# Kernel optimization log

Hardware: AMD Instinct MI355X
Metric: run time of the kernel (lower is better)

## Reference

```python
import jax, jax.numpy as jnp
import numpy as np


def setup_inputs() -> dict:
    key = jax.random.key(0)
    k1, k2, k3 = jax.random.split(key, 3)
    B, S, H = 32, 2048, 1024
    hidden = jax.random.normal(k1, (B, H), dtype=jnp.float32)
    encoder_outputs = jax.random.normal(k2, (B, S, H), dtype=jnp.float32)
    W_in = jax.random.normal(k3, (H, H), dtype=jnp.float32) * (1.0 / np.sqrt(H))
    return {"hidden": hidden, "encoder_outputs": encoder_outputs, "W_in": W_in}


def reference(hidden, encoder_outputs, W_in):
    # linear_in: nn.Linear(H, H, bias=False) -> hidden @ W_in.T  [B, H]
    h = hidden @ W_in.T
    # scores: bmm(encoder_outputs [B,S,H], h [B,H,1]) -> [B,S]
    scores = jnp.einsum("bsh,bh->bs", encoder_outputs, h)
    attn_w = jax.nn.softmax(scores, axis=-1)  # [B, S]
    # context: bmm(attn_w [B,1,S], encoder_outputs [B,S,H]) -> [B, H]
    context = jnp.einsum("bs,bsh->bh", attn_w, encoder_outputs)
    return (context, attn_w)
```

## Files before the change

kernel.cpp:

```cpp
#include <hip/hip_runtime.h>
#include <math.h>

constexpr int Bb = 32;
constexpr int Ss = 2048;
constexpr int Hh = 1024;
constexpr int SC = 64;
constexpr int CPB = Ss / SC;
constexpr int NBLK = Bb * CPB;

__global__ __launch_bounds__(256) void gemv_h_kernel(const float* __restrict__ hidden,
                                                     const float* __restrict__ W,
                                                     float* __restrict__ h)
{
    int tid  = threadIdx.x;
    int wave = tid >> 6;
    int lane = tid & 63;
    int i  = blockIdx.x & (Hh - 1);
    int bg = blockIdx.x >> 10;
    int b  = bg * 4 + wave;
    const float4* wr = reinterpret_cast<const float4*>(W + (size_t)i * Hh);
    const float4* hd = reinterpret_cast<const float4*>(hidden + (size_t)b * Hh);
    float d = 0.f;
#pragma unroll
    for (int k = 0; k < 4; ++k) {
        float4 wv = wr[lane + 64 * k];
        float4 hv = hd[lane + 64 * k];
        d += wv.x * hv.x + wv.y * hv.y + wv.z * hv.z + wv.w * hv.w;
    }
#pragma unroll
    for (int off = 32; off > 0; off >>= 1) d += __shfl_xor(d, off, 64);
    if (lane == 0) h[(size_t)b * Hh + i] = d;
}

__global__ __launch_bounds__(256) void attn_partial_kernel(const float* __restrict__ enc,
                                                           const float* __restrict__ h,
                                                           float* __restrict__ scores,
                                                           float* __restrict__ pm,
                                                           float* __restrict__ pl,
                                                           float* __restrict__ pctx)
{
    int blk   = blockIdx.x;
    int b     = blk / CPB;
    int chunk = blk % CPB;
    int s0    = chunk * SC;
    int tid   = threadIdx.x;
    int wave  = tid >> 6;
    int lane  = tid & 63;

    float4 hf[4];
    const float4* h4 = reinterpret_cast<const float4*>(h + (size_t)b * Hh);
#pragma unroll
    for (int k = 0; k < 4; ++k) hf[k] = h4[lane + 64 * k];

    float m = -INFINITY;
    float l = 0.f;
    float4 ctx[4];
#pragma unroll
    for (int k = 0; k < 4; ++k) ctx[k] = make_float4(0.f, 0.f, 0.f, 0.f);

    const float4* ebase = reinterpret_cast<const float4*>(enc + ((size_t)b * Ss + s0 + wave * 16) * Hh);

#pragma unroll 2
    for (int r2 = 0; r2 < 8; ++r2) {
        const float4* eA = ebase + (size_t)(2 * r2) * (Hh / 4);
        const float4* eB = eA + (Hh / 4);
        float4 ea[4], eb[4];
#pragma unroll
        for (int k = 0; k < 4; ++k) ea[k] = eA[lane + 64 * k];
#pragma unroll
        for (int k = 0; k < 4; ++k) eb[k] = eB[lane + 64 * k];

        float d0 = 0.f, d1 = 0.f;
#pragma unroll
        for (int k = 0; k < 4; ++k) {
            d0 += ea[k].x * hf[k].x + ea[k].y * hf[k].y + ea[k].z * hf[k].z + ea[k].w * hf[k].w;
            d1 += eb[k].x * hf[k].x + eb[k].y * hf[k].y + eb[k].z * hf[k].z + eb[k].w * hf[k].w;
        }
#pragma unroll
        for (int off = 32; off > 0; off >>= 1) {
            d0 += __shfl_xor(d0, off, 64);
            d1 += __shfl_xor(d1, off, 64);
        }
        int s = s0 + wave * 16 + 2 * r2;
        if (lane == 0) {
            *reinterpret_cast<float2*>(scores + (size_t)b * Ss + s) = make_float2(d0, d1);
        }

        float mn = fmaxf(fmaxf(d0, d1), m);
        if (mn > m) {
            float c = __expf(m - mn);
            l *= c;
#pragma unroll
            for (int k = 0; k < 4; ++k) {
                ctx[k].x *= c; ctx[k].y *= c; ctx[k].z *= c; ctx[k].w *= c;
            }
            m = mn;
        }
        float p0 = __expf(d0 - m);
        float p1 = __expf(d1 - m);
        l += p0 + p1;
#pragma unroll
        for (int k = 0; k < 4; ++k) {
            ctx[k].x += p0 * ea[k].x + p1 * eb[k].x;
            ctx[k].y += p0 * ea[k].y + p1 * eb[k].y;
            ctx[k].z += p0 * ea[k].z + p1 * eb[k].z;
            ctx[k].w += p0 * ea[k].w + p1 * eb[k].w;
        }
    }

    __shared__ float lds_ctx[4][Hh];
    __shared__ float lds_m[4], lds_l[4];
    float4* ldsrow = reinterpret_cast<float4*>(lds_ctx[wave]);
#pragma unroll
    for (int k = 0; k < 4; ++k) ldsrow[64 * k + lane] = ctx[k];
    if (lane == 0) { lds_m[wave] = m; lds_l[wave] = l; }
    __syncthreads();

    float M = fmaxf(fmaxf(lds_m[0], lds_m[1]), fmaxf(lds_m[2], lds_m[3]));
    float L = 0.f;
    float4 acc = make_float4(0.f, 0.f, 0.f, 0.f);
#pragma unroll
    for (int w = 0; w < 4; ++w) {
        float c = __expf(lds_m[w] - M);
        L += c * lds_l[w];
        float4 v = reinterpret_cast<float4*>(lds_ctx[w])[tid];
        acc.x += c * v.x; acc.y += c * v.y; acc.z += c * v.z; acc.w += c * v.w;
    }
    reinterpret_cast<float4*>(pctx + (size_t)blk * Hh)[tid] = acc;
    if (tid == 0) { pm[blk] = M; pl[blk] = L; }
}

__global__ __launch_bounds__(256) void combine_finish_kernel(const float* __restrict__ pm,
                                                             const float* __restrict__ pl,
                                                             const float* __restrict__ pctx,
                                                             const float* __restrict__ scores,
                                                             float* __restrict__ out_ctx,
                                                             float* __restrict__ attn_out)
{
    int blk = blockIdx.x;
    int tid = threadIdx.x;
    if (blk < 128) {
        int b = blk >> 2;
        int col = (blk & 3) * 256 + tid;
        const float* mrow = pm + (size_t)b * CPB;
        const float* lrow = pl + (size_t)b * CPB;
        float M = -INFINITY;
#pragma unroll
        for (int c = 0; c < CPB; ++c) M = fmaxf(M, mrow[c]);
        float e[CPB];
        float L = 0.f;
#pragma unroll
        for (int c = 0; c < CPB; ++c) {
            e[c] = __expf(mrow[c] - M);
            L += e[c] * lrow[c];
        }
        float acc = 0.f;
#pragma unroll 4
        for (int c = 0; c < CPB; ++c)
            acc += e[c] * pctx[((size_t)b * CPB + c) * Hh + col];
        out_ctx[(size_t)b * Hh + col] = acc / L;
    } else {
        int idx = (blk - 128) * 256 + tid;
        int b = idx >> 11;
        const float* mrow = pm + (size_t)b * CPB;
        const float* lrow = pl + (size_t)b * CPB;
        float M = -INFINITY;
#pragma unroll
        for (int c = 0; c < CPB; ++c) M = fmaxf(M, mrow[c]);
        float L = 0.f;
#pragma unroll
        for (int c = 0; c < CPB; ++c) L += __expf(mrow[c] - M) * lrow[c];
        attn_out[idx] = __expf(scores[idx] - M) / L;
    }
}

extern "C" void kernel_launch(void* const* d_in, const int* in_sizes, int n_in,
                              void* d_out, int out_size, void* d_ws, size_t ws_size,
                              hipStream_t stream) {
    const float* hidden = (const float*)d_in[0];
    const float* enc    = (const float*)d_in[1];
    const float* W_in   = (const float*)d_in[2];

    float* out_ctx  = (float*)d_out;
    float* out_attn = (float*)d_out + Bb * Hh;

    float* ws     = (float*)d_ws;
    float* h      = ws;
    float* scores = ws + 32768;
    float* pm     = ws + 98304;
    float* pl     = ws + 99328;
    float* pctx   = ws + 100352;
    (void)in_sizes; (void)n_in; (void)out_size; (void)ws_size;

    gemv_h_kernel<<<Hh * (Bb / 4), 256, 0, stream>>>(hidden, W_in, h);
    attn_partial_kernel<<<NBLK, 256, 0, stream>>>(enc, h, scores, pm, pl, pctx);
    combine_finish_kernel<<<128 + (Bb * Ss) / 256, 256, 0, stream>>>(pm, pl, pctx, scores,
                                                                     out_ctx, out_attn);
}
```

Baseline: 64.03 us.

## Double-buffer encoder row loads and double the sequence chunk per block

Each attention block now handles 128 sequence rows instead of 64, and each wave processes groups of 4 rows. A software pipeline ping-pongs between two register buffers so the next group's loads are in flight while the current group is computed. The aim is to hide memory latency on the bandwidth-bound encoder stream and halve the partial-context traffic for the combine step. The cost is much higher register pressure (32 float4 buffers), which may lower occupancy, and fewer blocks (512).

```diff
diff --git a/kernel.cpp b/kernel.cpp
--- a/kernel.cpp
+++ b/kernel.cpp
@@ -4,7 +4,7 @@
 constexpr int Bb = 32;
 constexpr int Ss = 2048;
 constexpr int Hh = 1024;
-constexpr int SC = 64;
+constexpr int SC = 128;
 constexpr int CPB = Ss / SC;
 constexpr int NBLK = Bb * CPB;
 
@@ -40,8 +40,8 @@
                                                            float* __restrict__ pctx)
 {
     int blk   = blockIdx.x;
-    int b     = blk / CPB;
-    int chunk = blk % CPB;
+    int b     = blk >> 4;
+    int chunk = blk & (CPB - 1);
     int s0    = chunk * SC;
     int tid   = threadIdx.x;
     int wave  = tid >> 6;
@@ -58,55 +58,79 @@
 #pragma unroll
     for (int k = 0; k < 4; ++k) ctx[k] = make_float4(0.f, 0.f, 0.f, 0.f);
 
-    const float4* ebase = reinterpret_cast<const float4*>(enc + ((size_t)b * Ss + s0 + wave * 16) * Hh);
-
-#pragma unroll 2
-    for (int r2 = 0; r2 < 8; ++r2) {
-        const float4* eA = ebase + (size_t)(2 * r2) * (Hh / 4);
-        const float4* eB = eA + (Hh / 4);
-        float4 ea[4], eb[4];
-#pragma unroll
-        for (int k = 0; k < 4; ++k) ea[k] = eA[lane + 64 * k];
-#pragma unroll
-        for (int k = 0; k < 4; ++k) eb[k] = eB[lane + 64 * k];
-
-        float d0 = 0.f, d1 = 0.f;
-#pragma unroll
-        for (int k = 0; k < 4; ++k) {
-            d0 += ea[k].x * hf[k].x + ea[k].y * hf[k].y + ea[k].z * hf[k].z + ea[k].w * hf[k].w;
-            d1 += eb[k].x * hf[k].x + eb[k].y * hf[k].y + eb[k].z * hf[k].z + eb[k].w * hf[k].w;
-        }
-#pragma unroll
-        for (int off = 32; off > 0; off >>= 1) {
-            d0 += __shfl_xor(d0, off, 64);
-            d1 += __shfl_xor(d1, off, 64);
-        }
-        int s = s0 + wave * 16 + 2 * r2;
-        if (lane == 0) {
-            *reinterpret_cast<float2*>(scores + (size_t)b * Ss + s) = make_float2(d0, d1);
-        }
-
-        float mn = fmaxf(fmaxf(d0, d1), m);
-        if (mn > m) {
-            float c = __expf(m - mn);
-            l *= c;
-#pragma unroll
-            for (int k = 0; k < 4; ++k) {
-                ctx[k].x *= c; ctx[k].y *= c; ctx[k].z *= c; ctx[k].w *= c;
-            }
-            m = mn;
-        }
-        float p0 = __expf(d0 - m);
-        float p1 = __expf(d1 - m);
-        l += p0 + p1;
-#pragma unroll
-        for (int k = 0; k < 4; ++k) {
-            ctx[k].x += p0 * ea[k].x + p1 * eb[k].x;
-            ctx[k].y += p0 * ea[k].y + p1 * eb[k].y;
-            ctx[k].z += p0 * ea[k].z + p1 * eb[k].z;
-            ctx[k].w += p0 * ea[k].w + p1 * eb[k].w;
-        }
-    }
+    const float4* ebase = reinterpret_cast<const float4*>(enc + ((size_t)b * Ss + s0 + wave * 32) * Hh);
+
+#define LOADQ(EV, Q)                                                        \
+    {                                                                       \
+        _Pragma("unroll")                                                   \
+        for (int r = 0; r < 4; ++r) {                                       \
+            const float4* e4 = ebase + (size_t)((Q) * 4 + r) * (Hh / 4);    \
+            _Pragma("unroll")                                               \
+            for (int k = 0; k < 4; ++k) EV[r][k] = e4[lane + 64 * k];       \
+        }                                                                   \
+    }
+
+#define COMPQ(EV, Q)                                                        \
+    {                                                                       \
+        float d[4];                                                         \
+        _Pragma("unroll")                                                   \
+        for (int r = 0; r < 4; ++r) {                                       \
+            d[r] = 0.f;                                                     \
+            _Pragma("unroll")                                               \
+            for (int k = 0; k < 4; ++k)                                     \
+                d[r] += EV[r][k].x * hf[k].x + EV[r][k].y * hf[k].y +       \
+                        EV[r][k].z * hf[k].z + EV[r][k].w * hf[k].w;        \
+        }                                                                   \
+        _Pragma("unroll")                                                   \
+        for (int off = 32; off > 0; off >>= 1) {                            \
+            _Pragma("unroll")                                               \
+            for (int r = 0; r < 4; ++r) d[r] += __shfl_xor(d[r], off, 64);  \
+        }                                                                   \
+        if (lane == 0) {                                                    \
+            *reinterpret_cast<float4*>(scores + (size_t)b * Ss + s0 +       \
+                                       wave * 32 + 4 * (Q)) =               \
+                make_float4(d[0], d[1], d[2], d[3]);                        \
+        }                                                                   \
+        float mn = fmaxf(fmaxf(fmaxf(d[0], d[1]), fmaxf(d[2], d[3])), m);   \
+        if (mn > m) {                                                       \
+            float c = __expf(m - mn);                                       \
+            l *= c;                                                         \
+            _Pragma("unroll")                                               \
+            for (int k = 0; k < 4; ++k) {                                   \
+                ctx[k].x *= c; ctx[k].y *= c; ctx[k].z *= c; ctx[k].w *= c; \
+            }                                                               \
+            m = mn;                                                         \
+        }                                                                   \
+        float p[4];                                                         \
+        _Pragma("unroll")                                                   \
+        for (int r = 0; r < 4; ++r) p[r] = __expf(d[r] - m);                \
+        l += (p[0] + p[1]) + (p[2] + p[3]);                                 \
+        _Pragma("unroll")                                                   \
+        for (int k = 0; k < 4; ++k) {                                       \
+            _Pragma("unroll")                                               \
+            for (int r = 0; r < 4; ++r) {                                   \
+                ctx[k].x += p[r] * EV[r][k].x;                              \
+                ctx[k].y += p[r] * EV[r][k].y;                              \
+                ctx[k].z += p[r] * EV[r][k].z;                              \
+                ctx[k].w += p[r] * EV[r][k].w;                              \
+            }                                                               \
+        }                                                                   \
+    }
+
+    float4 evA[4][4], evB[4][4];
+    LOADQ(evA, 0);
+#pragma unroll 1
+    for (int qq = 0; qq < 3; ++qq) {
+        LOADQ(evB, 2 * qq + 1);
+        COMPQ(evA, 2 * qq);
+        LOADQ(evA, 2 * qq + 2);
+        COMPQ(evB, 2 * qq + 1);
+    }
+    LOADQ(evB, 7);
+    COMPQ(evA, 6);
+    COMPQ(evB, 7);
+#undef LOADQ
+#undef COMPQ
 
     __shared__ float lds_ctx[4][Hh];
     __shared__ float lds_m[4], lds_l[4];
@@ -188,8 +212,8 @@
     float* h      = ws;
     float* scores = ws + 32768;
     float* pm     = ws + 98304;
-    float* pl     = ws + 99328;
-    float* pctx   = ws + 100352;
+    float* pl     = ws + 98816;
+    float* pctx   = ws + 99328;
     (void)in_sizes; (void)n_in; (void)out_size; (void)ws_size;
 
     gemv_h_kernel<<<Hh * (Bb / 4), 256, 0, stream>>>(hidden, W_in, h);
```

After: 59.84 us (median of 2 runs). -6.5%, faster.
